# Kernel optimization log

Measured on AMD Instinct MI355X. Metric: run time of the kernel, lower is better.

The kernel has to match this reference:

```python
import jax, jax.numpy as jnp
import numpy as np

N_NODES, N_EDGES = 100000, 1000000
NODE_IN, EDGE_IN, D_MODEL = 128, 64, 128


def setup_inputs() -> dict:
    key = jax.random.key(0)
    k1, k2, k3, k4, k5 = jax.random.split(key, 5)
    x_node = jax.random.normal(k1, (N_NODES, NODE_IN), dtype=jnp.float32)
    x_edge = jax.random.normal(k2, (N_EDGES, EDGE_IN), dtype=jnp.float32)
    edge_index = jax.random.randint(k3, (2, N_EDGES), 0, N_NODES, dtype=jnp.int64)
    # learned params (PyTorch Linear: y = x @ W.T + b)
    s_e = 1.0 / np.sqrt(EDGE_IN)
    s_n = 1.0 / np.sqrt(NODE_IN)
    W_edge = jax.random.uniform(k4, (D_MODEL, EDGE_IN), jnp.float32, -s_e, s_e)
    b_edge = jnp.zeros((D_MODEL,), jnp.float32)
    W_node = jax.random.uniform(k5, (D_MODEL, NODE_IN), jnp.float32, -s_n, s_n)
    b_node = jnp.zeros((D_MODEL,), jnp.float32)
    ln_gamma = jnp.ones((D_MODEL,), jnp.float32)
    ln_beta = jnp.zeros((D_MODEL,), jnp.float32)
    return {
        "x_node": x_node, "x_edge": x_edge, "edge_index": edge_index,
        "W_edge": W_edge, "b_edge": b_edge,
        "W_node": W_node, "b_node": b_node,
        "ln_gamma": ln_gamma, "ln_beta": ln_beta,
    }


def _layernorm(x, gamma, beta, eps=1e-5):
    mu = jnp.mean(x, axis=-1, keepdims=True)
    var = jnp.mean(jnp.square(x - mu), axis=-1, keepdims=True)
    return (x - mu) * jax.lax.rsqrt(var + eps) * gamma + beta


def reference(x_node, x_edge, edge_index, W_edge, b_edge, W_node, b_node, ln_gamma, ln_beta):
    src, dst = edge_index[0], edge_index[1]
    h_edge = x_edge @ W_edge.T + b_edge                       # [E, D]
    h_node = x_node @ W_node.T + b_node                       # [N, D] project once, then gather
    h_endpoints = (h_node[src] + h_node[dst]) * 0.5           # [E, D]
    return _layernorm(h_edge + h_endpoints, ln_gamma, ln_beta)
```

## Files before the change

### kernel.cpp

```cpp
#include <hip/hip_runtime.h>


typedef __attribute__((ext_vector_type(8))) short bf16x8;
typedef __attribute__((ext_vector_type(4))) float f32x4;

__device__ __forceinline__ short f2bf(float f) {
  unsigned u = __float_as_uint(f);
  u = (u + 0x7FFFu + ((u >> 16) & 1u)) >> 16;
  return (short)u;
}
__device__ __forceinline__ float bf2f(short s) {
  return __uint_as_float(((unsigned)(unsigned short)s) << 16);
}
__device__ __forceinline__ bf16x8 cvt8(const float* __restrict__ p) {
  const f32x4 a = *(const f32x4*)p;
  const f32x4 b = *(const f32x4*)(p + 4);
  bf16x8 r;
  r[0] = f2bf(a[0]); r[1] = f2bf(a[1]); r[2] = f2bf(a[2]); r[3] = f2bf(a[3]);
  r[4] = f2bf(b[0]); r[5] = f2bf(b[1]); r[6] = f2bf(b[2]); r[7] = f2bf(b[3]);
  return r;
}

__global__ __launch_bounds__(256) void node_mfma_kernel(
    const float* __restrict__ x_node,
    const float* __restrict__ W_node,
    const float* __restrict__ b_node,
    short* __restrict__ h_node,
    int n_nodes)
{
  const int lane = threadIdx.x & 63;
  const int c = lane & 15, g = lane >> 4;
  const int gw = blockIdx.x * 4 + (threadIdx.x >> 6);
  const int nw = gridDim.x * 4;
  const int ntiles = (n_nodes + 15) >> 4;

  bf16x8 aW[8][4];
#pragma unroll
  for (int t = 0; t < 8; ++t)
#pragma unroll
    for (int s = 0; s < 4; ++s)
      aW[t][s] = cvt8(W_node + (size_t)(16 * t + c) * 128 + 32 * s + 8 * g);

  for (int tile = gw; tile < ntiles; tile += nw) {
    const int n0 = tile << 4;
    const int n = (n0 + c < n_nodes) ? n0 + c : n_nodes - 1;
    const float* xr = x_node + (size_t)n * 128;
    bf16x8 bx[4];
#pragma unroll
    for (int s = 0; s < 4; ++s) bx[s] = cvt8(xr + 32 * s + 8 * g);

    f32x4 acc[8];
#pragma unroll
    for (int t = 0; t < 8; ++t)
      acc[t] = *(const f32x4*)(b_node + 16 * t + 4 * g);
#pragma unroll
    for (int t = 0; t < 8; ++t)
#pragma unroll
      for (int s = 0; s < 4; ++s)
        acc[t] = __builtin_amdgcn_mfma_f32_16x16x32_bf16(aW[t][s], bx[s], acc[t], 0, 0, 0);

    if (n0 + c < n_nodes) {
      short* o = h_node + (size_t)(n0 + c) * 128 + g * 32;
#pragma unroll
      for (int k = 0; k < 4; ++k) {
        bf16x8 v;
#pragma unroll
        for (int j = 0; j < 4; ++j) {
          v[j]     = f2bf(acc[2 * k][j]);
          v[4 + j] = f2bf(acc[2 * k + 1][j]);
        }
        *(bf16x8*)(o + 8 * k) = v;
      }
    }
  }
}

__global__ __launch_bounds__(256) void edge_mfma_kernel(
    const float* __restrict__ x_edge,
    const int*   __restrict__ eidx,
    const float* __restrict__ W_edge,
    const float* __restrict__ b_edge,
    const short* __restrict__ h_node,
    const float* __restrict__ gamma,
    const float* __restrict__ beta,
    float* __restrict__ out,
    int n_edges)
{
  const int lane = threadIdx.x & 63;
  const int c = lane & 15, g = lane >> 4;
  const int gw = blockIdx.x * 4 + (threadIdx.x >> 6);
  const int nw = gridDim.x * 4;
  const int ntiles = (n_edges + 15) >> 4;

  bf16x8 aW[8][2];
#pragma unroll
  for (int t = 0; t < 8; ++t)
#pragma unroll
    for (int s = 0; s < 2; ++s)
      aW[t][s] = cvt8(W_edge + (size_t)(16 * t + c) * 64 + 32 * s + 8 * g);

  int tile = gw;
  bf16x8 bx0, bx1;
  int src = 0, dst = 0;
  if (tile < ntiles) {
    const int e = (tile * 16 + c < n_edges) ? tile * 16 + c : n_edges - 1;
    const float* xr = x_edge + (size_t)e * 64;
    bx0 = cvt8(xr + 8 * g);
    bx1 = cvt8(xr + 32 + 8 * g);
    src = eidx[e];
    dst = eidx[n_edges + e];
  }

  for (; tile < ntiles; tile += nw) {
    const short* hs = h_node + (size_t)src * 128 + g * 32;
    const short* hd = h_node + (size_t)dst * 128 + g * 32;
    bf16x8 vs[4], vd[4];
#pragma unroll
    for (int k = 0; k < 4; ++k) {
      vs[k] = *(const bf16x8*)(hs + 8 * k);
      vd[k] = *(const bf16x8*)(hd + 8 * k);
    }

    const int ntile = (tile + nw < ntiles) ? tile + nw : ntiles - 1;
    const int en = (ntile * 16 + c < n_edges) ? ntile * 16 + c : n_edges - 1;
    const float* xrn = x_edge + (size_t)en * 64;
    const bf16x8 bxn0 = cvt8(xrn + 8 * g);
    const bf16x8 bxn1 = cvt8(xrn + 32 + 8 * g);
    const int srcn = eidx[en];
    const int dstn = eidx[n_edges + en];

    f32x4 acc[8];
#pragma unroll
    for (int t = 0; t < 8; ++t)
      acc[t] = *(const f32x4*)(b_edge + 16 * t + 4 * g);
#pragma unroll
    for (int t = 0; t < 8; ++t) {
      acc[t] = __builtin_amdgcn_mfma_f32_16x16x32_bf16(aW[t][0], bx0, acc[t], 0, 0, 0);
      acc[t] = __builtin_amdgcn_mfma_f32_16x16x32_bf16(aW[t][1], bx1, acc[t], 0, 0, 0);
    }

#pragma unroll
    for (int k = 0; k < 4; ++k)
#pragma unroll
      for (int j = 0; j < 4; ++j) {
        acc[2 * k][j]     += 0.5f * (bf2f(vs[k][j])     + bf2f(vd[k][j]));
        acc[2 * k + 1][j] += 0.5f * (bf2f(vs[k][4 + j]) + bf2f(vd[k][4 + j]));
      }

    float s1 = 0.f;
#pragma unroll
    for (int t = 0; t < 8; ++t)
      s1 += (acc[t][0] + acc[t][1]) + (acc[t][2] + acc[t][3]);
    s1 += __shfl_xor(s1, 16, 64);
    s1 += __shfl_xor(s1, 32, 64);
    const float mu = s1 * (1.f / 128.f);

    float s2 = 0.f;
#pragma unroll
    for (int t = 0; t < 8; ++t)
#pragma unroll
      for (int j = 0; j < 4; ++j) {
        const float d = acc[t][j] - mu;
        acc[t][j] = d;
        s2 = fmaf(d, d, s2);
      }
    s2 += __shfl_xor(s2, 16, 64);
    s2 += __shfl_xor(s2, 32, 64);
    const float rstd = rsqrtf(s2 * (1.f / 128.f) + 1e-5f);

    const int e0 = tile << 4;
    if (e0 + c < n_edges) {
      float* o = out + (size_t)(e0 + c) * 128 + 4 * g;
#pragma unroll
      for (int t = 0; t < 8; ++t) {
        const f32x4 gg = *(const f32x4*)(gamma + 16 * t + 4 * g);
        const f32x4 be = *(const f32x4*)(beta + 16 * t + 4 * g);
        f32x4 r;
#pragma unroll
        for (int j = 0; j < 4; ++j) r[j] = fmaf(acc[t][j] * rstd, gg[j], be[j]);
        *(f32x4*)(o + 16 * t) = r;
      }
    }

    bx0 = bxn0; bx1 = bxn1; src = srcn; dst = dstn;
  }
}

extern "C" void kernel_launch(void* const* d_in, const int* in_sizes, int n_in,
                              void* d_out, int out_size, void* d_ws, size_t ws_size,
                              hipStream_t stream) {
  const float* x_node = (const float*)d_in[0];
  const float* x_edge = (const float*)d_in[1];
  const int*   eidx   = (const int*)  d_in[2];
  const float* W_edge = (const float*)d_in[3];
  const float* b_edge = (const float*)d_in[4];
  const float* W_node = (const float*)d_in[5];
  const float* b_node = (const float*)d_in[6];
  const float* gamma  = (const float*)d_in[7];
  const float* beta   = (const float*)d_in[8];
  float* out = (float*)d_out;

  const int n_nodes = in_sizes[0] / 128;
  const int n_edges = in_sizes[2] / 2;

  short* h_node = (short*)d_ws;
  if (ws_size < (size_t)n_nodes * 128 * sizeof(short)) return;

  node_mfma_kernel<<<512, 256, 0, stream>>>(x_node, W_node, b_node, h_node, n_nodes);
  edge_mfma_kernel<<<2048, 256, 0, stream>>>(x_edge, eidx, W_edge, b_edge,
                                             h_node, gamma, beta, out, n_edges);
}
```

Before: 295.3 us.

## Stage edge weights in LDS and double-buffer gather prefetch in edge kernel

The edge kernel now converts W_edge to bf16 once per block and keeps it in swizzled shared memory. Bias, gamma and beta also go to shared memory instead of being held in registers or reloaded from global memory. The main loop becomes a two-slot software pipeline: the h_node gathers for the next tile and the index and x_edge loads for the tile after that are issued while the current tile is computed. The aim is to hide the latency of the random gathers and to free registers for deeper prefetching. The cost is extra LDS reads per MFMA and a more complex loop with more live prefetch registers.

New measurement: 275.8 us. 1.07x faster.

```diff
diff --git a/kernel.cpp b/kernel.cpp
--- a/kernel.cpp
+++ b/kernel.cpp
@@ -86,67 +86,76 @@
     float* __restrict__ out,
     int n_edges)
 {
+  __shared__ short Wlds[8192];
+  __shared__ float plds[384];
+
+  const int tid = threadIdx.x;
+  {
+    const int r = tid >> 1, h = tid & 1;
+    const float* wr = W_edge + (size_t)r * 64 + 32 * h;
+#pragma unroll
+    for (int q = 0; q < 4; ++q) {
+      const bf16x8 v = cvt8(wr + 8 * q);
+      const int slot = (4 * h + q) ^ (r & 7);
+      *(bf16x8*)(&Wlds[r * 64 + slot * 8]) = v;
+    }
+    if (tid < 128) {
+      plds[tid]       = b_edge[tid];
+      plds[128 + tid] = gamma[tid];
+      plds[256 + tid] = beta[tid];
+    }
+  }
+  __syncthreads();
+
   const int lane = threadIdx.x & 63;
   const int c = lane & 15, g = lane >> 4;
   const int gw = blockIdx.x * 4 + (threadIdx.x >> 6);
   const int nw = gridDim.x * 4;
   const int ntiles = (n_edges + 15) >> 4;
 
-  bf16x8 aW[8][2];
-#pragma unroll
-  for (int t = 0; t < 8; ++t)
-#pragma unroll
-    for (int s = 0; s < 2; ++s)
-      aW[t][s] = cvt8(W_edge + (size_t)(16 * t + c) * 64 + 32 * s + 8 * g);
-
-  int tile = gw;
-  bf16x8 bx0, bx1;
-  int src = 0, dst = 0;
-  if (tile < ntiles) {
+  const int w0off = c * 64 + ((g) ^ (c & 7)) * 8;
+  const int w1off = c * 64 + ((4 + g) ^ (c & 7)) * 8;
+
+  if (gw >= ntiles) return;
+
+  auto LOADIDX = [&](int tile, int& src, int& dst) {
+    const int e = (tile * 16 + c < n_edges) ? tile * 16 + c : n_edges - 1;
+    src = eidx[e];
+    dst = eidx[n_edges + e];
+  };
+  auto LOADX = [&](int tile, bf16x8& b0, bf16x8& b1) {
     const int e = (tile * 16 + c < n_edges) ? tile * 16 + c : n_edges - 1;
     const float* xr = x_edge + (size_t)e * 64;
-    bx0 = cvt8(xr + 8 * g);
-    bx1 = cvt8(xr + 32 + 8 * g);
-    src = eidx[e];
-    dst = eidx[n_edges + e];
-  }
-
-  for (; tile < ntiles; tile += nw) {
+    b0 = cvt8(xr + 8 * g);
+    b1 = cvt8(xr + 32 + 8 * g);
+  };
+  auto GATHER = [&](int src, int dst, bf16x8* vs, bf16x8* vd) {
     const short* hs = h_node + (size_t)src * 128 + g * 32;
     const short* hd = h_node + (size_t)dst * 128 + g * 32;
-    bf16x8 vs[4], vd[4];
 #pragma unroll
     for (int k = 0; k < 4; ++k) {
       vs[k] = *(const bf16x8*)(hs + 8 * k);
       vd[k] = *(const bf16x8*)(hd + 8 * k);
     }
-
-    const int ntile = (tile + nw < ntiles) ? tile + nw : ntiles - 1;
-    const int en = (ntile * 16 + c < n_edges) ? ntile * 16 + c : n_edges - 1;
-    const float* xrn = x_edge + (size_t)en * 64;
-    const bf16x8 bxn0 = cvt8(xrn + 8 * g);
-    const bf16x8 bxn1 = cvt8(xrn + 32 + 8 * g);
-    const int srcn = eidx[en];
-    const int dstn = eidx[n_edges + en];
-
+  };
+  auto COMPUTE = [&](int tile, bf16x8 b0, bf16x8 b1, bf16x8* vs, bf16x8* vd) {
     f32x4 acc[8];
 #pragma unroll
-    for (int t = 0; t < 8; ++t)
-      acc[t] = *(const f32x4*)(b_edge + 16 * t + 4 * g);
+    for (int k = 0; k < 4; ++k)
+#pragma unroll
+      for (int j = 0; j < 4; ++j) {
+        acc[2 * k][j]     = plds[16 * (2 * k) + 4 * g + j]
+                          + 0.5f * (bf2f(vs[k][j]) + bf2f(vd[k][j]));
+        acc[2 * k + 1][j] = plds[16 * (2 * k + 1) + 4 * g + j]
+                          + 0.5f * (bf2f(vs[k][4 + j]) + bf2f(vd[k][4 + j]));
+      }
 #pragma unroll
     for (int t = 0; t < 8; ++t) {
-      acc[t] = __builtin_amdgcn_mfma_f32_16x16x32_bf16(aW[t][0], bx0, acc[t], 0, 0, 0);
-      acc[t] = __builtin_amdgcn_mfma_f32_16x16x32_bf16(aW[t][1], bx1, acc[t], 0, 0, 0);
-    }
-
-#pragma unroll
-    for (int k = 0; k < 4; ++k)
-#pragma unroll
-      for (int j = 0; j < 4; ++j) {
-        acc[2 * k][j]     += 0.5f * (bf2f(vs[k][j])     + bf2f(vd[k][j]));
-        acc[2 * k + 1][j] += 0.5f * (bf2f(vs[k][4 + j]) + bf2f(vd[k][4 + j]));
-      }
-
+      const bf16x8 a0 = *(const bf16x8*)(&Wlds[t * 1024 + w0off]);
+      const bf16x8 a1 = *(const bf16x8*)(&Wlds[t * 1024 + w1off]);
+      acc[t] = __builtin_amdgcn_mfma_f32_16x16x32_bf16(a0, b0, acc[t], 0, 0, 0);
+      acc[t] = __builtin_amdgcn_mfma_f32_16x16x32_bf16(a1, b1, acc[t], 0, 0, 0);
+    }
     float s1 = 0.f;
 #pragma unroll
     for (int t = 0; t < 8; ++t)
@@ -168,21 +177,45 @@
     s2 += __shfl_xor(s2, 32, 64);
     const float rstd = rsqrtf(s2 * (1.f / 128.f) + 1e-5f);
 
-    const int e0 = tile << 4;
-    if (e0 + c < n_edges) {
-      float* o = out + (size_t)(e0 + c) * 128 + 4 * g;
+    if (tile * 16 + c < n_edges) {
+      float* o = out + (size_t)(tile * 16 + c) * 128 + 4 * g;
 #pragma unroll
       for (int t = 0; t < 8; ++t) {
-        const f32x4 gg = *(const f32x4*)(gamma + 16 * t + 4 * g);
-        const f32x4 be = *(const f32x4*)(beta + 16 * t + 4 * g);
         f32x4 r;
 #pragma unroll
-        for (int j = 0; j < 4; ++j) r[j] = fmaf(acc[t][j] * rstd, gg[j], be[j]);
+        for (int j = 0; j < 4; ++j)
+          r[j] = fmaf(acc[t][j] * rstd, plds[128 + 16 * t + 4 * g + j],
+                      plds[256 + 16 * t + 4 * g + j]);
         *(f32x4*)(o + 16 * t) = r;
       }
     }
-
-    bx0 = bxn0; bx1 = bxn1; src = srcn; dst = dstn;
+  };
+
+  bf16x8 bxA0, bxA1, bxB0, bxB1;
+  bf16x8 vsA[4], vdA[4], vsB[4], vdB[4];
+  int srcA, dstA, srcB, dstB;
+
+  LOADIDX(gw, srcA, dstA);
+  LOADX(gw, bxA0, bxA1);
+  GATHER(srcA, dstA, vsA, vdA);
+  LOADIDX(gw + nw, srcB, dstB);
+  LOADX(gw + nw, bxB0, bxB1);
+
+  int t = gw;
+  for (;;) {
+    GATHER(srcB, dstB, vsB, vdB);
+    LOADIDX(t + 2 * nw, srcA, dstA);
+    COMPUTE(t, bxA0, bxA1, vsA, vdA);
+    LOADX(t + 2 * nw, bxA0, bxA1);
+    t += nw;
+    if (t >= ntiles) break;
+
+    GATHER(srcA, dstA, vsA, vdA);
+    LOADIDX(t + 2 * nw, srcB, dstB);
+    COMPUTE(t, bxB0, bxB1, vsB, vdB);
+    LOADX(t + 2 * nw, bxB0, bxB1);
+    t += nw;
+    if (t >= ntiles) break;
   }
 }
 
```
